# Kernel optimization log

Measured on AMD Instinct MI355X. Metric: run time of the kernel, lower is better.

Reference implementation:

```python
import jax, jax.numpy as jnp
import numpy as np

W_SEG = 2048   # segment_length w
R = 4          # dilation r
H = 16         # num_attention_heads


def setup_inputs() -> dict:
    key = jax.random.key(0)
    k0, k1, k2 = jax.random.split(key, 3)
    B, S, Hid = 2, 8192, 1024
    X = jax.random.normal(k0, (B, S, Hid), dtype=jnp.float32)
    Wq = jax.random.normal(k1, (Hid, Hid), dtype=jnp.float32) * 0.02
    bq = jnp.zeros((Hid,), jnp.float32)
    Wkv = jax.random.normal(k2, (Hid, 2 * Hid), dtype=jnp.float32) * 0.02
    bkv = jnp.zeros((2 * Hid,), jnp.float32)
    return {"X": X, "Wq": Wq, "bq": bq, "Wkv": Wkv, "bkv": bkv}


def reference(X, Wq, bq, Wkv, bkv):
    B, S, Hid = X.shape
    D = Hid // H                      # head dim
    num_points = W_SEG // R           # tokens kept per segment
    num_seg = S // W_SEG
    scale = 1.0 / np.sqrt(D).astype(np.float32)

    q = (X @ Wq + bq).reshape(B, S, H, D)
    kv = (X @ Wkv + bkv).reshape(B, S, 2, H, D)
    k, v = kv[:, :, 0], kv[:, :, 1]

    # dilated base indices: segment offset + r-strided points -> [num_seg*num_points]
    base = (jnp.arange(num_seg)[:, None] * W_SEG
            + jnp.arange(num_points)[None, :] * R).reshape(-1)
    shift = jnp.arange(H) % R                       # per-head shift
    idx = base[None, :] + shift[:, None]            # [H, T']
    Tq = idx.shape[1]
    idxT = idx.T                                    # [T', H]
    head_ix = jnp.arange(H)[None, :]                # [1, H] -> broadcasts with idxT

    # per-head dilated gather: sparse[b, t, h, d] = full[b, idx[h, t], h, d]
    sq = q[:, idxT, head_ix, :]                     # [B, T', H, D]
    sk = k[:, idxT, head_ix, :]
    sv = v[:, idxT, head_ix, :]

    sq = sq.reshape(B, num_seg, num_points, H, D)
    sk = sk.reshape(B, num_seg, num_points, H, D)
    sv = sv.reshape(B, num_seg, num_points, H, D)

    # per-segment (non-causal) attention, same math as flash_attn_kvpacked_func
    scores = jnp.einsum('bsqhd,bskhd->bshqk', sq, sk) * scale
    probs = jax.nn.softmax(scores, axis=-1)
    ctx = jnp.einsum('bshqk,bskhd->bsqhd', probs, sv)
    ctx = ctx.reshape(B, Tq, H, D)

    # scatter back into zeros at the gathered positions (unique per head)
    out = jnp.zeros((B, S, H, D), ctx.dtype).at[:, idxT, head_ix, :].set(ctx)
    return out.reshape(B, S, Hid)
```

## Files before the change

kernel.cpp:

```cpp
#include <hip/hip_runtime.h>

typedef unsigned short u16;
typedef unsigned int   u32;
typedef __bf16 bf16x8 __attribute__((ext_vector_type(8)));
typedef float  f32x4  __attribute__((ext_vector_type(4)));
typedef short  s16x4  __attribute__((ext_vector_type(4)));

#define QSCALE 0.125f

__device__ __forceinline__ u16 f2bf(float f) {
  union { float f; u32 u; } a; a.f = f;
  u32 u = a.u;
  u = (u + 0x7FFFu + ((u >> 16) & 1u)) >> 16;
  return (u16)u;
}

__device__ __forceinline__ u32 pack2bf(float a, float b) {
  u32 xa = __float_as_uint(a) + 0x8000u;
  u32 xb = __float_as_uint(b) + 0x8000u;
  return __builtin_amdgcn_perm(xb, xa, 0x07060302u);
}

__device__ __forceinline__ void async16(const void* g, void* l) {
  __builtin_amdgcn_global_load_lds(
      (const __attribute__((address_space(1))) void*)g,
      (__attribute__((address_space(3))) void*)l, 16, 0, 0);
}

__global__ __launch_bounds__(256) void pack_x(const float* __restrict__ X,
                                              u16* __restrict__ Xp) {
  __shared__ u16 sh[4096];
  int bx = blockIdx.x;
  int ks = bx & 31, Mtile = (bx >> 5) & 31, r = bx >> 10;
  int tid = threadIdx.x;
  int rl = tid >> 1, half = tid & 1;
  int mt = rl >> 4, mm = rl & 15;
  int srow = (Mtile >> 2) * 2048 + ((Mtile & 3) * 128 + rl) * 4 + r;
  const float* s0 = X + (size_t)srow * 1024 + ks * 32 + half * 16;
  float4 a0 = *(const float4*)(s0);
  float4 a1 = *(const float4*)(s0 + 4);
  float4 a2 = *(const float4*)(s0 + 8);
  float4 a3 = *(const float4*)(s0 + 12);
  uint4 c0, c1;
  c0.x = pack2bf(a0.x, a0.y); c0.y = pack2bf(a0.z, a0.w);
  c0.z = pack2bf(a1.x, a1.y); c0.w = pack2bf(a1.z, a1.w);
  c1.x = pack2bf(a2.x, a2.y); c1.y = pack2bf(a2.z, a2.w);
  c1.z = pack2bf(a3.x, a3.y); c1.w = pack2bf(a3.z, a3.w);
  int base = (mt * 64 + mm) * 8 + half * 256;
  *(uint4*)&sh[base] = c0;
  *(uint4*)&sh[base + 128] = c1;
  __syncthreads();
  u16* dst = Xp + (size_t)bx * 4096 + tid * 16;
  uint4 d0 = *(const uint4*)&sh[tid * 16];
  uint4 d1 = *(const uint4*)&sh[tid * 16 + 8];
  *(uint4*)(dst) = d0;
  *(uint4*)(dst + 8) = d1;
}

__global__ __launch_bounds__(256) void pack_w(const float* __restrict__ Wq,
                                              const float* __restrict__ Wkv,
                                              u16* __restrict__ Wp,
                                              const float* __restrict__ bq,
                                              const float* __restrict__ bkv,
                                              float* __restrict__ bp) {
  __shared__ float tile[32][65];
  int bx = blockIdx.x;
  if (bx >= 1536) {
    int idx = (bx - 1536) * 256 + threadIdx.x;
    int r = idx / 768, n = idx % 768;
    int t = n >> 8, hh = (n >> 6) & 3, d = n & 63;
    int h = hh * 4 + r;
    float v = (t == 0) ? bq[h * 64 + d] * QSCALE
            : (t == 1) ? bkv[h * 64 + d]
                       : bkv[1024 + h * 64 + d];
    bp[idx] = v;
    return;
  }
  int ks = bx & 31; int rem = bx >> 5;
  int hh = rem & 3; rem >>= 2;
  int t  = rem % 3; int r = rem / 3;
  int h  = hh * 4 + r;
  const float* src; int rs, cb;
  if (t == 0)      { src = Wq;  rs = 1024; cb = h * 64; }
  else if (t == 1) { src = Wkv; rs = 2048; cb = h * 64; }
  else             { src = Wkv; rs = 2048; cb = 1024 + h * 64; }
  int tid = threadIdx.x;
  {
    int kk = tid >> 3, dd = (tid & 7) << 3;
    const float* s0 = src + (size_t)(ks * 32 + kk) * rs + cb + dd;
    float4 a = *(const float4*)s0;
    float4 c = *(const float4*)(s0 + 4);
    tile[kk][dd + 0] = a.x; tile[kk][dd + 1] = a.y;
    tile[kk][dd + 2] = a.z; tile[kk][dd + 3] = a.w;
    tile[kk][dd + 4] = c.x; tile[kk][dd + 5] = c.y;
    tile[kk][dd + 6] = c.z; tile[kk][dd + 7] = c.w;
  }
  __syncthreads();
  {
    int d = tid >> 2, kc = tid & 3;
    float sc = (t == 0) ? QSCALE : 1.0f;
    u32 w[4];
#pragma unroll
    for (int j = 0; j < 4; ++j) {
      u16 lo = f2bf(tile[kc * 8 + 2 * j][d] * sc);
      u16 hi = f2bf(tile[kc * 8 + 2 * j + 1][d] * sc);
      w[j] = (u32)lo | ((u32)hi << 16);
    }
    int n = t * 256 + hh * 64 + d;
    int Nt = n >> 7, nt = (n >> 4) & 7, nn = n & 15;
    size_t off = (size_t)r * 786432 + (size_t)Nt * 131072 +
                 (size_t)ks * 4096 + nt * 512 + kc * 128 + nn * 8;
    uint4 o; o.x = w[0]; o.y = w[1]; o.z = w[2]; o.w = w[3];
    *(uint4*)(Wp + off) = o;
  }
}

__global__ __launch_bounds__(256, 3) void gemm1(const u16* __restrict__ Ap,
                                                const u16* __restrict__ Wp,
                                                const float* __restrict__ bp,
                                                u16* __restrict__ Qd,
                                                u16* __restrict__ Kd,
                                                u16* __restrict__ Vd) {
  __shared__ u16 lds[16384];
  u16* bufA0 = lds;
  u16* bufA1 = lds + 4096;
  u16* bufB0 = lds + 8192;
  u16* bufB1 = lds + 12288;
  int bx = blockIdx.x;
  int xcd = bx & 7;
  int idx = bx >> 3;
  int r = xcd >> 1;
  int Mtile = (xcd & 1) * 16 + (idx / 6);
  int Ntile = idx % 6;
  int tid = threadIdx.x, w = tid >> 6, lane = tid & 63;
  int wr = w >> 1, wc = w & 1;
  int l15 = lane & 15, l4 = lane >> 4;

  const u16* Aw = Ap + (size_t)(r * 32 + Mtile) * 131072 + w * 1024 + lane * 8;
  const u16* Bw = Wp + (size_t)r * 786432 + (size_t)Ntile * 131072 +
                  w * 1024 + lane * 8;

  async16(Aw,       &bufA0[w * 1024]);
  async16(Aw + 512, &bufA0[w * 1024 + 512]);
  async16(Bw,       &bufB0[w * 1024]);
  async16(Bw + 512, &bufB0[w * 1024 + 512]);

  f32x4 acc[4][4] = {};
  for (int ks = 0; ks < 32; ++ks) {
    u16* bA = (ks & 1) ? bufA1 : bufA0;
    u16* bB = (ks & 1) ? bufB1 : bufB0;
    __syncthreads();
    if (ks < 31) {
      u16* nA = (ks & 1) ? bufA0 : bufA1;
      u16* nB = (ks & 1) ? bufB0 : bufB1;
      const u16* a = Aw + (ks + 1) * 4096;
      const u16* b = Bw + (ks + 1) * 4096;
      async16(a,       &nA[w * 1024]);
      async16(a + 512, &nA[w * 1024 + 512]);
      async16(b,       &nB[w * 1024]);
      async16(b + 512, &nB[w * 1024 + 512]);
    }
    bf16x8 af[4], bf[4];
#pragma unroll
    for (int i = 0; i < 4; ++i)
      af[i] = *(const bf16x8*)&bA[((wr * 4 + i) * 64 + lane) * 8];
#pragma unroll
    for (int j = 0; j < 4; ++j)
      bf[j] = *(const bf16x8*)&bB[((wc * 4 + j) * 64 + lane) * 8];
#pragma unroll
    for (int i = 0; i < 4; ++i)
#pragma unroll
      for (int j = 0; j < 4; ++j)
        acc[i][j] = __builtin_amdgcn_mfma_f32_16x16x32_bf16(af[i], bf[j],
                                                            acc[i][j], 0, 0, 0);
  }

  int nb = Ntile * 128 + wc * 64;
  int t = nb >> 8, hh = (nb >> 6) & 3;
  int h = hh * 4 + r;
  u16* T = (t == 0) ? Qd : ((t == 1) ? Kd : Vd);
  float biasv[4];
#pragma unroll
  for (int j = 0; j < 4; ++j) biasv[j] = bp[r * 768 + nb + j * 16 + l15];

  u16* eb = lds + w * 1152;
  int rrow = lane >> 2, seg = lane & 3;
#pragma unroll
  for (int i = 0; i < 4; ++i) {
    __syncthreads();
#pragma unroll
    for (int j = 0; j < 4; ++j)
#pragma unroll
      for (int reg = 0; reg < 4; ++reg)
        eb[(l4 * 4 + reg) * 72 + j * 16 + l15] = f2bf(acc[i][j][reg] + biasv[j]);
    __syncthreads();
    uint4 d0 = *(const uint4*)&eb[rrow * 72 + seg * 16];
    uint4 d1 = *(const uint4*)&eb[rrow * 72 + seg * 16 + 8];
    int m = Mtile * 128 + wr * 64 + i * 16 + rrow;
    int bseg = m >> 9, p = m & 511;
    size_t off = ((size_t)(bseg * 16 + h) * 512 + p) * 64 + seg * 16;
    *(uint4*)(T + off) = d0;
    *(uint4*)(T + off + 8) = d1;
  }
}

__global__ __launch_bounds__(512, 4) void attn(const u16* __restrict__ Qd,
                                               const u16* __restrict__ Kd,
                                               const u16* __restrict__ Vd,
                                               float* __restrict__ out) {
  __shared__ u16 ldsK[128 * 72];
  __shared__ u16 ldsV[64 * 136];
  int bx = blockIdx.x;
  int unit = bx & 127, qq = bx >> 7;
  int b = unit >> 6, seg = (unit >> 4) & 3, h = unit & 15;
  int tid = threadIdx.x, w = tid >> 6, lane = tid & 63;
  int l15 = lane & 15, l4 = lane >> 4;
  const u16* Qu = Qd + (size_t)unit * 32768;
  const u16* Ku = Kd + (size_t)unit * 32768;
  const u16* Vu = Vd + (size_t)unit * 32768;

  int q0 = qq * 128 + w * 16;
  bf16x8 qf[2];
#pragma unroll
  for (int hf = 0; hf < 2; ++hf)
    qf[hf] = *(const bf16x8*)(Qu + (q0 + l15) * 64 + hf * 32 + l4 * 8);

  f32x4 O[4] = {};
  float lrun = 0.f;

  int c0 = tid, c1 = 512 + tid;
  int kp0 = c0 >> 3, kd0 = c0 & 7;
  int kp1 = c1 >> 3, kd1 = c1 & 7;
  int vd0 = (c0 & 7) << 3, vd1 = (c1 & 7) << 3;

  uint4 kreg0 = *(const uint4*)(Ku + c0 * 8);
  uint4 kreg1 = *(const uint4*)(Ku + c1 * 8);
  uint4 vreg0 = *(const uint4*)(Vu + c0 * 8);
  uint4 vreg1 = *(const uint4*)(Vu + c1 * 8);

  for (int ch = 0; ch < 4; ++ch) {
    __syncthreads();
    *(uint4*)&ldsK[kp0 * 72 + kd0 * 8] = kreg0;
    *(uint4*)&ldsK[kp1 * 72 + kd1 * 8] = kreg1;
    {
      u32 ww0[4] = {vreg0.x, vreg0.y, vreg0.z, vreg0.w};
      u32 ww1[4] = {vreg1.x, vreg1.y, vreg1.z, vreg1.w};
#pragma unroll
      for (int j = 0; j < 4; ++j) {
        ldsV[(vd0 + 2 * j) * 136 + kp0]     = (u16)(ww0[j] & 0xFFFFu);
        ldsV[(vd0 + 2 * j + 1) * 136 + kp0] = (u16)(ww0[j] >> 16);
        ldsV[(vd1 + 2 * j) * 136 + kp1]     = (u16)(ww1[j] & 0xFFFFu);
        ldsV[(vd1 + 2 * j + 1) * 136 + kp1] = (u16)(ww1[j] >> 16);
      }
    }
    __syncthreads();
    if (ch < 3) {
      const u16* Ksn = Ku + (ch + 1) * 8192;
      const u16* Vsn = Vu + (ch + 1) * 8192;
      kreg0 = *(const uint4*)(Ksn + c0 * 8);
      kreg1 = *(const uint4*)(Ksn + c1 * 8);
      vreg0 = *(const uint4*)(Vsn + c0 * 8);
      vreg1 = *(const uint4*)(Vsn + c1 * 8);
    }

    float csum = 0.f;
    s16x4 pk[8];
#pragma unroll
    for (int kt = 0; kt < 8; ++kt) {
      bf16x8 a0 = *(const bf16x8*)&ldsK[(kt * 16 + l15) * 72 + l4 * 8];
      bf16x8 a1 = *(const bf16x8*)&ldsK[(kt * 16 + l15) * 72 + 32 + l4 * 8];
      f32x4 s = __builtin_amdgcn_mfma_f32_16x16x32_bf16(
          a0, qf[0], (f32x4){0.f, 0.f, 0.f, 0.f}, 0, 0, 0);
      s = __builtin_amdgcn_mfma_f32_16x16x32_bf16(a1, qf[1], s, 0, 0, 0);
      float e0 = __expf(s[0]);
      float e1 = __expf(s[1]);
      float e2 = __expf(s[2]);
      float e3 = __expf(s[3]);
      csum += (e0 + e1) + (e2 + e3);
      s16x4 pv;
      pv[0] = (short)(__float_as_uint(e0) >> 16);
      pv[1] = (short)(__float_as_uint(e1) >> 16);
      pv[2] = (short)(__float_as_uint(e2) >> 16);
      pv[3] = (short)(__float_as_uint(e3) >> 16);
      pk[kt] = pv;
    }
    csum += __shfl_xor(csum, 16, 64);
    csum += __shfl_xor(csum, 32, 64);
    lrun += csum;
#pragma unroll
    for (int kt = 0; kt < 8; ++kt)
#pragma unroll
      for (int dn = 0; dn < 4; ++dn) {
        s16x4 vb = *(const s16x4*)&ldsV[(dn * 16 + l15) * 136 + kt * 16 + l4 * 4];
        O[dn] = __builtin_amdgcn_mfma_f32_16x16x16bf16_1k(pk[kt], vb,
                                                          O[dn], 0, 0, 0);
      }
  }

  {
    float rl = __builtin_amdgcn_rcpf(lrun);
#pragma unroll
    for (int reg = 0; reg < 4; ++reg) {
      float rr = __shfl(rl, l4 * 4 + reg, 64);
      int p = q0 + l4 * 4 + reg;
      int spos = seg * 2048 + p * 4 + (h & 3);
      size_t base = ((size_t)(b * 8192 + spos)) * 1024 + h * 64 + l15;
#pragma unroll
      for (int dn = 0; dn < 4; ++dn)
        out[base + dn * 16] = O[dn][reg] * rr;
    }
  }

  {
    int row_i = bx * 32 + (tid >> 4);
    int sub = tid & 15;
    int rr = row_i & 3;
    float4 z = {0.f, 0.f, 0.f, 0.f};
    float* rowp = out + (size_t)row_i * 1024 + sub * 4;
#pragma unroll
    for (int hz = 0; hz < 16; ++hz) {
      if ((hz & 3) == rr) continue;
      *(float4*)(rowp + hz * 64) = z;
    }
  }
}

extern "C" void kernel_launch(void* const* d_in, const int* in_sizes, int n_in,
                              void* d_out, int out_size, void* d_ws, size_t ws_size,
                              hipStream_t stream) {
  (void)in_sizes; (void)n_in; (void)ws_size; (void)out_size;
  const float* X   = (const float*)d_in[0];
  const float* Wq  = (const float*)d_in[1];
  const float* bq  = (const float*)d_in[2];
  const float* Wkv = (const float*)d_in[3];
  const float* bkv = (const float*)d_in[4];
  float* out = (float*)d_out;
  char* ws = (char*)d_ws;
  u16*  Wp = (u16*)(ws);
  float* bp = (float*)(ws + 6291456);
  u16*  Qd = (u16*)(ws + 6303744);
  u16*  Kd = (u16*)(ws + 14692352);
  u16*  Vd = (u16*)(ws + 23080960);
  u16*  Xp = (u16*)d_out;

  pack_x <<<4096, 256, 0, stream>>>(X, Xp);
  pack_w <<<1548, 256, 0, stream>>>(Wq, Wkv, Wp, bq, bkv, bp);
  gemm1  <<<768,  256, 0, stream>>>(Xp, Wp, bp, Qd, Kd, Vd);
  attn   <<<512,  512, 0, stream>>>(Qd, Kd, Vd, out);
}
```

Baseline: 186.0 us.

## Store V transposed from projection GEMM to remove scalar LDS transpose in attention

```diff
diff --git a/kernel.cpp b/kernel.cpp
--- a/kernel.cpp
+++ b/kernel.cpp
@@ -178,22 +178,41 @@
   int nb = Ntile * 128 + wc * 64;
   int t = nb >> 8, hh = (nb >> 6) & 3;
   int h = hh * 4 + r;
-  u16* T = (t == 0) ? Qd : ((t == 1) ? Kd : Vd);
   float biasv[4];
 #pragma unroll
   for (int j = 0; j < 4; ++j) biasv[j] = bp[r * 768 + nb + j * 16 + l15];
 
+  if (t == 2) {
+#pragma unroll
+    for (int i = 0; i < 4; ++i) {
+      int m = Mtile * 128 + wr * 64 + i * 16 + l4 * 4;
+      int bseg = m >> 9, p = m & 511;
+      size_t ub = (size_t)(bseg * 16 + h) * 32768;
+#pragma unroll
+      for (int j = 0; j < 4; ++j) {
+        int d = j * 16 + l15;
+        s16x4 o;
+        o[0] = (short)f2bf(acc[i][j][0] + biasv[j]);
+        o[1] = (short)f2bf(acc[i][j][1] + biasv[j]);
+        o[2] = (short)f2bf(acc[i][j][2] + biasv[j]);
+        o[3] = (short)f2bf(acc[i][j][3] + biasv[j]);
+        *(s16x4*)(Vd + ub + d * 512 + p) = o;
+      }
+    }
+    return;
+  }
+
+  u16* T = (t == 0) ? Qd : Kd;
   u16* eb = lds + w * 1152;
   int rrow = lane >> 2, seg = lane & 3;
+  __syncthreads();
 #pragma unroll
   for (int i = 0; i < 4; ++i) {
-    __syncthreads();
 #pragma unroll
     for (int j = 0; j < 4; ++j)
 #pragma unroll
       for (int reg = 0; reg < 4; ++reg)
         eb[(l4 * 4 + reg) * 72 + j * 16 + l15] = f2bf(acc[i][j][reg] + biasv[j]);
-    __syncthreads();
     uint4 d0 = *(const uint4*)&eb[rrow * 72 + seg * 16];
     uint4 d1 = *(const uint4*)&eb[rrow * 72 + seg * 16 + 8];
     int m = Mtile * 128 + wr * 64 + i * 16 + rrow;
@@ -231,36 +250,28 @@
   int c0 = tid, c1 = 512 + tid;
   int kp0 = c0 >> 3, kd0 = c0 & 7;
   int kp1 = c1 >> 3, kd1 = c1 & 7;
-  int vd0 = (c0 & 7) << 3, vd1 = (c1 & 7) << 3;
+  int vr0 = c0 >> 4, vc0 = (c0 & 15) << 3;
+  int vr1 = c1 >> 4, vc1 = (c1 & 15) << 3;
 
   uint4 kreg0 = *(const uint4*)(Ku + c0 * 8);
   uint4 kreg1 = *(const uint4*)(Ku + c1 * 8);
-  uint4 vreg0 = *(const uint4*)(Vu + c0 * 8);
-  uint4 vreg1 = *(const uint4*)(Vu + c1 * 8);
+  uint4 vreg0 = *(const uint4*)(Vu + vr0 * 512 + vc0);
+  uint4 vreg1 = *(const uint4*)(Vu + vr1 * 512 + vc1);
 
   for (int ch = 0; ch < 4; ++ch) {
     __syncthreads();
     *(uint4*)&ldsK[kp0 * 72 + kd0 * 8] = kreg0;
     *(uint4*)&ldsK[kp1 * 72 + kd1 * 8] = kreg1;
-    {
-      u32 ww0[4] = {vreg0.x, vreg0.y, vreg0.z, vreg0.w};
-      u32 ww1[4] = {vreg1.x, vreg1.y, vreg1.z, vreg1.w};
-#pragma unroll
-      for (int j = 0; j < 4; ++j) {
-        ldsV[(vd0 + 2 * j) * 136 + kp0]     = (u16)(ww0[j] & 0xFFFFu);
-        ldsV[(vd0 + 2 * j + 1) * 136 + kp0] = (u16)(ww0[j] >> 16);
-        ldsV[(vd1 + 2 * j) * 136 + kp1]     = (u16)(ww1[j] & 0xFFFFu);
-        ldsV[(vd1 + 2 * j + 1) * 136 + kp1] = (u16)(ww1[j] >> 16);
-      }
-    }
+    *(uint4*)&ldsV[vr0 * 136 + vc0] = vreg0;
+    *(uint4*)&ldsV[vr1 * 136 + vc1] = vreg1;
     __syncthreads();
     if (ch < 3) {
       const u16* Ksn = Ku + (ch + 1) * 8192;
-      const u16* Vsn = Vu + (ch + 1) * 8192;
+      const u16* Vsn = Vu + (ch + 1) * 128;
       kreg0 = *(const uint4*)(Ksn + c0 * 8);
       kreg1 = *(const uint4*)(Ksn + c1 * 8);
-      vreg0 = *(const uint4*)(Vsn + c0 * 8);
-      vreg1 = *(const uint4*)(Vsn + c1 * 8);
+      vreg0 = *(const uint4*)(Vsn + vr0 * 512 + vc0);
+      vreg1 = *(const uint4*)(Vsn + vr1 * 512 + vc1);
     }
 
     float csum = 0.f;
```

Measured after the change: 183.9 us. No clear change (-1.1%).
